# Performance work log

Measured on AMD Instinct MI355X. Metric: run time of the kernel, lower is better.

## Reference

```python
import jax, jax.numpy as jnp
import numpy as np

S = 128      # number of segments
F = 256      # in_features
H = 128      # mlp hidden


def setup_inputs() -> dict:
    key = jax.random.key(0)
    k1, k2, k3 = jax.random.split(key, 3)
    rng = np.random.default_rng(0)
    lengths = rng.integers(1024, 3073, size=S).astype(np.int32)  # ragged segment sizes
    N = int(lengths.sum())  # ~262144 total tokens
    x = jax.random.normal(k1, (N, F), dtype=jnp.float32)
    W1 = jax.random.normal(k2, (F, H), dtype=jnp.float32) * (1.0 / np.sqrt(F))
    b1 = jnp.zeros((H,), dtype=jnp.float32)
    W2 = jax.random.normal(k3, (H, 2), dtype=jnp.float32) * (1.0 / np.sqrt(H))
    b2 = jnp.zeros((2,), dtype=jnp.float32)
    return {"x": x, "lengths": jnp.asarray(lengths), "W1": W1, "b1": b1, "W2": W2, "b2": b2}


def reference(x, lengths, W1, b1, W2, b2):
    N = x.shape[0]
    nseg = lengths.shape[0]
    seg_ids = jnp.repeat(jnp.arange(nseg), lengths, total_repeat_length=N)  # [N]
    offsets = jnp.concatenate([jnp.zeros((1,), lengths.dtype), jnp.cumsum(lengths)[:-1]])
    # position within segment: arange(1, L+1) / L
    pos = (jnp.arange(N) - offsets[seg_ids] + 1).astype(x.dtype)
    Lf = lengths.astype(x.dtype)
    xpos = pos / Lf[seg_ids]  # [N]

    # MLP: Linear -> Tanh -> Linear
    ms = jnp.tanh(x @ W1 + b1) @ W2 + b2  # [N, 2]
    y, z = ms[:, 0], ms[:, 1]

    # per-segment softmax-weighted mean of positions (calc_mean)
    ymax = jax.ops.segment_max(y, seg_ids, num_segments=nseg)
    w = jnp.exp(y - ymax[seg_ids])
    wsum = jax.ops.segment_sum(w, seg_ids, num_segments=nseg)
    means = jax.ops.segment_sum(xpos * w, seg_ids, num_segments=nseg) / wsum  # [S]

    # per-segment softplus(mean(z))
    stds = jax.nn.softplus(jax.ops.segment_sum(z, seg_ids, num_segments=nseg) / Lf)  # [S]

    # normal pdf weights per token
    mu = means[seg_ids]
    sd = stds[seg_ids]
    inv_sqrt_2pi = 1.0 / jnp.sqrt(2.0 * jnp.pi).astype(x.dtype)
    pdf = jnp.exp(-0.5 * ((xpos - mu) / sd) ** 2) * (inv_sqrt_2pi / sd)  # [N]

    # normalize per segment with +0.001 stabilizer
    psum = jax.ops.segment_sum(pdf, seg_ids, num_segments=nseg)
    attn = (pdf / (psum[seg_ids] + 0.001))[:, None]  # [N, 1]

    # attention-weighted sum of features per segment
    out = jax.ops.segment_sum(attn * x, seg_ids, num_segments=nseg)  # [S, F]
    return out, attn
```

## Files before the change

kernel.cpp:

```cpp
#include <hip/hip_runtime.h>
#include <math.h>

#define F 256
#define Hh 128
#define MAXL 3072

typedef short bf16x8 __attribute__((ext_vector_type(8)));
typedef float f32x4 __attribute__((ext_vector_type(4)));
typedef unsigned int uint4v __attribute__((ext_vector_type(4)));

__device__ inline unsigned short f2bf_rne(float f) {
  unsigned u = __float_as_uint(f);
  unsigned r = u + 0x7fff + ((u >> 16) & 1);
  return (unsigned short)(r >> 16);
}
__device__ inline float bf2f(unsigned short h) {
  return __uint_as_float((unsigned)h << 16);
}

__global__ void init_kernel(const int* __restrict__ lengths, int* __restrict__ offsets,
                            float* __restrict__ out, const float* __restrict__ W1,
                            unsigned short* __restrict__ whT, unsigned short* __restrict__ wlT,
                            int S, int outN) {
  int t = blockIdx.x * blockDim.x + threadIdx.x;
  int stride = gridDim.x * blockDim.x;
  for (int i = t; i < outN; i += stride) out[i] = 0.f;
  for (int i = t; i < F * Hh; i += stride) {
    int k = i >> 7, col = i & 127;
    float v = W1[i];
    unsigned short h = f2bf_rne(v);
    unsigned short l = f2bf_rne(v - bf2f(h));
    int dst = (k >> 5) * (128 * 32) + col * 32 + (k & 31);
    whT[dst] = h;
    wlT[dst] = l;
  }
  if (blockIdx.x == 0) {
    __shared__ int buf[256];
    int tid = threadIdx.x;
    int v = (tid < S) ? lengths[tid] : 0;
    buf[tid] = v;
    __syncthreads();
    for (int o = 1; o < 256; o <<= 1) {
      int add = (tid >= o) ? buf[tid - o] : 0;
      __syncthreads();
      buf[tid] += add;
      __syncthreads();
    }
    if (tid < S) offsets[tid] = buf[tid] - v;
    if (tid == S - 1) offsets[S] = buf[tid];
  }
}

#define STAGE(B, KC) do {                                               \
    _Pragma("unroll")                                                   \
    for (int r = 0; r < 4; ++r) {                                       \
      __builtin_amdgcn_global_load_lds(                                 \
          (const __attribute__((address_space(1))) unsigned int*)       \
              (srow[r] + (KC) * 32),                                    \
          (__attribute__((address_space(3))) unsigned int*)             \
              (xs + (B) * 4096 + r * 1024 + t * 4),                     \
          16, 0, 0);                                                    \
    }                                                                   \
  } while (0)

#define SPLIT_MFMA(V0, V1, RT) do {                                     \
    float f[8] = {V0.x, V0.y, V0.z, V0.w, V1.x, V1.y, V1.z, V1.w};      \
    union { uint4v u; bf16x8 b; } ah, al;                               \
    _Pragma("unroll")                                                   \
    for (int q = 0; q < 4; ++q) {                                       \
      unsigned ua = __float_as_uint(f[2 * q]);                          \
      unsigned ub = __float_as_uint(f[2 * q + 1]);                      \
      ah.u[q] = __builtin_amdgcn_perm(ub, ua, 0x07060302u);             \
      float ra = f[2 * q]     - __uint_as_float(ua & 0xFFFF0000u);      \
      float rb = f[2 * q + 1] - __uint_as_float(ub & 0xFFFF0000u);      \
      al.u[q] = __builtin_amdgcn_perm(__float_as_uint(rb),              \
                                      __float_as_uint(ra),              \
                                      0x07060302u);                     \
    }                                                                   \
    _Pragma("unroll")                                                   \
    for (int ct = 0; ct < 4; ++ct) {                                    \
      acc[RT][ct] = __builtin_amdgcn_mfma_f32_16x16x32_bf16(            \
          ah.b, bh[ct], acc[RT][ct], 0, 0, 0);                          \
      acc[RT][ct] = __builtin_amdgcn_mfma_f32_16x16x32_bf16(            \
          ah.b, bl[ct], acc[RT][ct], 0, 0, 0);                          \
      acc[RT][ct] = __builtin_amdgcn_mfma_f32_16x16x32_bf16(            \
          al.b, bh[ct], acc[RT][ct], 0, 0, 0);                          \
    }                                                                   \
  } while (0)

__global__ __launch_bounds__(256) void mlp_kernel(
    const float* __restrict__ x,
    const unsigned short* __restrict__ whT, const unsigned short* __restrict__ wlT,
    const float* __restrict__ b1, const float* __restrict__ W2,
    const float* __restrict__ b2, float* __restrict__ yv,
    float* __restrict__ zv, int N) {
  __shared__ float xs[2 * 4096];
  __shared__ float redy[128][2];
  __shared__ float redz[128][2];

  const int t = threadIdx.x;
  const int lane = t & 63;
  const int w = t >> 6;
  const int wr = w >> 1, wc = w & 1;
  const int ln15 = lane & 15, lq = lane >> 4;

  const int row0 = blockIdx.x * 128;

  f32x4 acc[4][4];
#pragma unroll
  for (int i = 0; i < 4; ++i)
#pragma unroll
    for (int j = 0; j < 4; ++j) acc[i][j] = (f32x4){0.f, 0.f, 0.f, 0.f};

  const float* srow[4];
  {
    const int rsub = t >> 3;
    const int swzs = (rsub & 7) << 4;
    const int scolb = ((t & 7) * 16) ^ swzs;
#pragma unroll
    for (int r = 0; r < 4; ++r) {
      int grow = row0 + r * 32 + rsub;
      grow = grow < N ? grow : N - 1;
      srow[r] = x + (size_t)grow * F + (scolb >> 2);
    }
  }

  const int row_l = wr * 64 + ln15;
  const int swzr = (ln15 & 7) << 4;
  const int p0base = row_l * 128 + ((lq * 32) ^ swzr);

  const int cbase = wc * 64 + ln15;
  const unsigned short* wb = whT + cbase * 32 + lq * 8;
  const unsigned short* lb = wlT + cbase * 32 + lq * 8;

  STAGE(0, 0);

#pragma unroll
  for (int kc = 0; kc < 8; ++kc) {
    bf16x8 bh[4], bl[4];
#pragma unroll
    for (int ct = 0; ct < 4; ++ct) {
      bh[ct] = *(const bf16x8*)(wb + kc * 4096 + ct * 512);
      bl[ct] = *(const bf16x8*)(lb + kc * 4096 + ct * 512);
    }
    if (kc < 7) STAGE((kc + 1) & 1, kc + 1);

    asm volatile("s_waitcnt vmcnt(4)" ::: "memory");
    asm volatile("s_barrier" ::: "memory");

    const char* bufp = (const char*)xs + (kc & 1) * 16384;
#pragma unroll
    for (int rt = 0; rt < 4; ++rt) {
      const int p0 = p0base + rt * 2048;
      float4 lo = *(const float4*)(bufp + p0);
      float4 hi = *(const float4*)(bufp + (p0 ^ 16));
      SPLIT_MFMA(lo, hi, rt);
    }
    asm volatile("s_barrier" ::: "memory");
  }

  float yp[4][4], zp[4][4];
#pragma unroll
  for (int i = 0; i < 4; ++i)
#pragma unroll
    for (int j = 0; j < 4; ++j) { yp[i][j] = 0.f; zp[i][j] = 0.f; }
#pragma unroll
  for (int ct = 0; ct < 4; ++ct) {
    int c = cbase + ct * 16;
    float b1c = b1[c], wyc = W2[2 * c], wzc = W2[2 * c + 1];
#pragma unroll
    for (int rt = 0; rt < 4; ++rt)
#pragma unroll
      for (int rg = 0; rg < 4; ++rg) {
        float a = acc[rt][ct][rg] + b1c;
        float e = __expf(2.f * a);
        float h = 1.f - __fdividef(2.f, e + 1.f);
        yp[rt][rg] = fmaf(h, wyc, yp[rt][rg]);
        zp[rt][rg] = fmaf(h, wzc, zp[rt][rg]);
      }
  }
#pragma unroll
  for (int rt = 0; rt < 4; ++rt)
#pragma unroll
    for (int rg = 0; rg < 4; ++rg) {
      float vy = yp[rt][rg], vz = zp[rt][rg];
#pragma unroll
      for (int m = 8; m; m >>= 1) {
        vy += __shfl_xor(vy, m);
        vz += __shfl_xor(vz, m);
      }
      if (ln15 == 0) {
        int row = wr * 64 + rt * 16 + lq * 4 + rg;
        redy[row][wc] = vy;
        redz[row][wc] = vz;
      }
    }
  __syncthreads();
  if (t < 128) {
    int g = row0 + t;
    if (g < N) {
      yv[g] = redy[t][0] + redy[t][1] + b2[0];
      zv[g] = redz[t][0] + redz[t][1] + b2[1];
    }
  }
}
#undef STAGE
#undef SPLIT_MFMA

__device__ inline float wave_reduce_sum(float v) {
#pragma unroll
  for (int o = 32; o; o >>= 1) v += __shfl_down(v, o);
  return v;
}
__device__ inline float wave_reduce_max(float v) {
#pragma unroll
  for (int o = 32; o; o >>= 1) v = fmaxf(v, __shfl_down(v, o));
  return v;
}

__global__ __launch_bounds__(256) void pool_kernel(
    const float* __restrict__ x,
    const float* __restrict__ yv, const float* __restrict__ zv,
    const int* __restrict__ offsets, const int* __restrict__ lengths,
    float* __restrict__ attn, float* __restrict__ out,
    int nchunks, int S) {
  __shared__ float ybuf[MAXL];
  __shared__ float4 sbuf[4][64];
  __shared__ float redA[4], redB[4], redC[4];

  const int s = S - 1 - blockIdx.y;
  const int c = nchunks - 1 - blockIdx.x;
  const int off = offsets[s], L = lengths[s];
  const int t = threadIdx.x;
  const int lane = t & 63, wid = t >> 6;

  float lmax = -1e30f;
  for (int i = t; i < L; i += 256) {
    float yy = yv[off + i];
    ybuf[i] = yy;
    lmax = fmaxf(lmax, yy);
  }
  lmax = wave_reduce_max(lmax);
  if (lane == 0) redA[wid] = lmax;
  __syncthreads();
  const float ymax = fmaxf(fmaxf(redA[0], redA[1]), fmaxf(redA[2], redA[3]));
  const float invL = 1.f / (float)L;
  __syncthreads();

  float sw = 0.f, smx = 0.f, sz = 0.f;
  for (int i = t; i < L; i += 256) {
    float wgt = __expf(ybuf[i] - ymax);
    float xp = (float)(i + 1) * invL;
    sw += wgt;
    smx = fmaf(xp, wgt, smx);
    sz += zv[off + i];
  }
  sw = wave_reduce_sum(sw);
  smx = wave_reduce_sum(smx);
  sz = wave_reduce_sum(sz);
  if (lane == 0) { redA[wid] = sw; redB[wid] = smx; redC[wid] = sz; }
  __syncthreads();
  const float wsum = (redA[0] + redA[1]) + (redA[2] + redA[3]);
  const float mxs  = (redB[0] + redB[1]) + (redB[2] + redB[3]);
  const float zsum = (redC[0] + redC[1]) + (redC[2] + redC[3]);
  const float mu = mxs / wsum;
  const float tz = zsum * invL;
  const float sd = fmaxf(tz, 0.f) + log1pf(__expf(-fabsf(tz)));
  const float invsd = 1.f / sd;
  const float Cg = 0.3989422804014327f;
  __syncthreads();

  float ps = 0.f;
  for (int i = t; i < L; i += 256) {
    float xp = (float)(i + 1) * invL;
    float u = (xp - mu) * invsd;
    ps += __expf(-0.5f * u * u);
  }
  ps = wave_reduce_sum(ps);
  if (lane == 0) redA[wid] = ps;
  __syncthreads();
  const float psum = ((redA[0] + redA[1]) + (redA[2] + redA[3])) * (Cg * invsd);
  const float scale = (Cg * invsd) / (psum + 0.001f);

  const int i0 = (int)((long long)L * c / nchunks);
  const int i1 = (int)((long long)L * (c + 1) / nchunks);
  for (int i = i0 + t; i < i1; i += 256) {
    float xp = (float)(i + 1) * invL;
    float u = (xp - mu) * invsd;
    attn[off + i] = __expf(-0.5f * u * u) * scale;
  }

  float4 a0 = make_float4(0.f, 0.f, 0.f, 0.f);
  float4 a1 = make_float4(0.f, 0.f, 0.f, 0.f);
  int i = i1 - 1 - wid;
  for (; i - 4 >= i0; i -= 8) {
    float xpa = (float)(i + 1) * invL;
    float ua = (xpa - mu) * invsd;
    float w0 = __expf(-0.5f * ua * ua) * scale;
    float xpb = (float)(i - 3) * invL;
    float ub = (xpb - mu) * invsd;
    float w1 = __expf(-0.5f * ub * ub) * scale;
    float4 v0 = *(const float4*)&x[(size_t)(off + i) * F + lane * 4];
    float4 v1 = *(const float4*)&x[(size_t)(off + i - 4) * F + lane * 4];
    a0.x = fmaf(w0, v0.x, a0.x); a0.y = fmaf(w0, v0.y, a0.y);
    a0.z = fmaf(w0, v0.z, a0.z); a0.w = fmaf(w0, v0.w, a0.w);
    a1.x = fmaf(w1, v1.x, a1.x); a1.y = fmaf(w1, v1.y, a1.y);
    a1.z = fmaf(w1, v1.z, a1.z); a1.w = fmaf(w1, v1.w, a1.w);
  }
  if (i >= i0) {
    float xpa = (float)(i + 1) * invL;
    float ua = (xpa - mu) * invsd;
    float w0 = __expf(-0.5f * ua * ua) * scale;
    float4 v0 = *(const float4*)&x[(size_t)(off + i) * F + lane * 4];
    a0.x = fmaf(w0, v0.x, a0.x); a0.y = fmaf(w0, v0.y, a0.y);
    a0.z = fmaf(w0, v0.z, a0.z); a0.w = fmaf(w0, v0.w, a0.w);
  }
  a0.x += a1.x; a0.y += a1.y; a0.z += a1.z; a0.w += a1.w;
  sbuf[wid][lane] = a0;
  __syncthreads();
  if (wid == 0) {
    float4 r0 = sbuf[0][lane], r1 = sbuf[1][lane];
    float4 r2 = sbuf[2][lane], r3 = sbuf[3][lane];
    float rx = (r0.x + r1.x) + (r2.x + r3.x);
    float ry = (r0.y + r1.y) + (r2.y + r3.y);
    float rz = (r0.z + r1.z) + (r2.z + r3.z);
    float rw = (r0.w + r1.w) + (r2.w + r3.w);
    float* o = &out[s * F + lane * 4];
    atomicAdd(o + 0, rx);
    atomicAdd(o + 1, ry);
    atomicAdd(o + 2, rz);
    atomicAdd(o + 3, rw);
  }
}

extern "C" void kernel_launch(void* const* d_in, const int* in_sizes, int n_in,
                              void* d_out, int out_size, void* d_ws, size_t ws_size,
                              hipStream_t stream) {
  const float* x      = (const float*)d_in[0];
  const int* lengths  = (const int*)d_in[1];
  const float* W1     = (const float*)d_in[2];
  const float* b1     = (const float*)d_in[3];
  const float* W2     = (const float*)d_in[4];
  const float* b2     = (const float*)d_in[5];
  const int S = in_sizes[1];
  const int N = in_sizes[0] / F;

  float* out  = (float*)d_out;
  float* attn = out + (size_t)S * F;

  int*   offsets = (int*)d_ws;
  float* yv = (float*)d_ws + 512;
  float* zv = yv + N;
  unsigned short* whT = (unsigned short*)(zv + N);
  unsigned short* wlT = whT + F * Hh;

  init_kernel<<<64, 256, 0, stream>>>(lengths, offsets, out, W1, whT, wlT, S, S * F);
  mlp_kernel<<<(N + 127) / 128, 256, 0, stream>>>(x, whT, wlT, b1, W2, b2, yv, zv, N);
  pool_kernel<<<dim3(8, S), 256, 0, stream>>>(x, yv, zv, offsets, lengths, attn, out, 8, S);
}
```

Baseline: 442.1 us.

## Triple-buffer x tiles in LDS and prefetch weight fragments one step ahead

The MLP kernel moves from double to triple buffering of the x tile in LDS, so global-to-LDS loads are issued two k-chunks ahead. The bf16 weight fragments are also loaded one iteration ahead into a two-slot register buffer. Wait counts are adjusted per iteration, and sched_barriers pin the issue order. This hides more global memory latency, at the cost of more LDS (48KB per block) and more VGPRs, which may lower occupancy.

```diff
diff --git a/kernel.cpp b/kernel.cpp
--- a/kernel.cpp
+++ b/kernel.cpp
@@ -63,7 +63,15 @@
     }                                                                   \
   } while (0)
 
-#define SPLIT_MFMA(V0, V1, RT) do {                                     \
+#define BLOAD(P, KC) do {                                               \
+    _Pragma("unroll")                                                   \
+    for (int ct = 0; ct < 4; ++ct) {                                    \
+      bh[P][ct] = *(const bf16x8*)(wb + (KC) * 4096 + ct * 512);        \
+      bl[P][ct] = *(const bf16x8*)(lb + (KC) * 4096 + ct * 512);        \
+    }                                                                   \
+  } while (0)
+
+#define SPLIT_MFMA(V0, V1, RT, P) do {                                  \
     float f[8] = {V0.x, V0.y, V0.z, V0.w, V1.x, V1.y, V1.z, V1.w};      \
     union { uint4v u; bf16x8 b; } ah, al;                               \
     _Pragma("unroll")                                                   \
@@ -80,11 +88,11 @@
     _Pragma("unroll")                                                   \
     for (int ct = 0; ct < 4; ++ct) {                                    \
       acc[RT][ct] = __builtin_amdgcn_mfma_f32_16x16x32_bf16(            \
-          ah.b, bh[ct], acc[RT][ct], 0, 0, 0);                          \
+          ah.b, bh[P][ct], acc[RT][ct], 0, 0, 0);                       \
       acc[RT][ct] = __builtin_amdgcn_mfma_f32_16x16x32_bf16(            \
-          ah.b, bl[ct], acc[RT][ct], 0, 0, 0);                          \
+          ah.b, bl[P][ct], acc[RT][ct], 0, 0, 0);                       \
       acc[RT][ct] = __builtin_amdgcn_mfma_f32_16x16x32_bf16(            \
-          al.b, bh[ct], acc[RT][ct], 0, 0, 0);                          \
+          al.b, bh[P][ct], acc[RT][ct], 0, 0, 0);                       \
     }                                                                   \
   } while (0)
 
@@ -94,7 +102,7 @@
     const float* __restrict__ b1, const float* __restrict__ W2,
     const float* __restrict__ b2, float* __restrict__ yv,
     float* __restrict__ zv, int N) {
-  __shared__ float xs[2 * 4096];
+  __shared__ float xs[3 * 4096];
   __shared__ float redy[128][2];
   __shared__ float redz[128][2];
 
@@ -133,28 +141,33 @@
   const unsigned short* wb = whT + cbase * 32 + lq * 8;
   const unsigned short* lb = wlT + cbase * 32 + lq * 8;
 
+  bf16x8 bh[2][4], bl[2][4];
+
+  BLOAD(0, 0);
+  __builtin_amdgcn_sched_barrier(0);
   STAGE(0, 0);
+  STAGE(1, 1);
+  __builtin_amdgcn_sched_barrier(0);
 
 #pragma unroll
   for (int kc = 0; kc < 8; ++kc) {
-    bf16x8 bh[4], bl[4];
-#pragma unroll
-    for (int ct = 0; ct < 4; ++ct) {
-      bh[ct] = *(const bf16x8*)(wb + kc * 4096 + ct * 512);
-      bl[ct] = *(const bf16x8*)(lb + kc * 4096 + ct * 512);
-    }
-    if (kc < 7) STAGE((kc + 1) & 1, kc + 1);
-
-    asm volatile("s_waitcnt vmcnt(4)" ::: "memory");
+    if (kc < 7) BLOAD((kc + 1) & 1, kc + 1);
+    __builtin_amdgcn_sched_barrier(0);
+    if (kc < 6) STAGE((kc + 2) % 3, kc + 2);
+    __builtin_amdgcn_sched_barrier(0);
+
+    if (kc < 6)       asm volatile("s_waitcnt vmcnt(16)" ::: "memory");
+    else if (kc == 6) asm volatile("s_waitcnt vmcnt(12)" ::: "memory");
+    else              asm volatile("s_waitcnt vmcnt(0)"  ::: "memory");
     asm volatile("s_barrier" ::: "memory");
 
-    const char* bufp = (const char*)xs + (kc & 1) * 16384;
+    const char* bufp = (const char*)xs + (kc % 3) * 16384;
 #pragma unroll
     for (int rt = 0; rt < 4; ++rt) {
       const int p0 = p0base + rt * 2048;
       float4 lo = *(const float4*)(bufp + p0);
       float4 hi = *(const float4*)(bufp + (p0 ^ 16));
-      SPLIT_MFMA(lo, hi, rt);
+      SPLIT_MFMA(lo, hi, rt, kc & 1);
     }
     asm volatile("s_barrier" ::: "memory");
   }
@@ -205,6 +218,7 @@
   }
 }
 #undef STAGE
+#undef BLOAD
 #undef SPLIT_MFMA
 
 __device__ inline float wave_reduce_sum(float v) {
```

Result: no change. 447.8 us (+1.3%).
